# Optimization experiments

Measured on AMD Instinct MI355X. Metric: run time of the kernel, lower is better.

The kernel has to match this reference:

```python
import jax, jax.numpy as jnp
import numpy as np

NW, NT, F, H = 8192, 4096, 128, 128


def setup_inputs() -> dict:
    key = jax.random.key(0)
    ks = jax.random.split(key, 16)
    s = 1.0 / np.sqrt(F)
    sh = 1.0 / np.sqrt(H)
    inp = {
        "raw_worker_x": jax.random.normal(ks[0], (NW, F), jnp.float32),
        "raw_task_x": jax.random.normal(ks[1], (NT, F), jnp.float32),
        # sparse binary adjacencies (p=0.01), stored dense as the module expects
        "ww_adj": (jax.random.uniform(ks[2], (NW, NW)) < 0.01).astype(jnp.float32),
        "wt_adj": (jax.random.uniform(ks[3], (NW, NT)) < 0.01).astype(jnp.float32),
        # projections (Linear with bias), stored [in, out]
        "Wp_w": jax.random.uniform(ks[4], (F, H), jnp.float32, -s, s),
        "bp_w": jax.random.uniform(ks[5], (H,), jnp.float32, -s, s),
        "Wp_t": jax.random.uniform(ks[6], (F, H), jnp.float32, -s, s),
        "bp_t": jax.random.uniform(ks[7], (H,), jnp.float32, -s, s),
        # RGCN layer
        "W_worker": jax.random.uniform(ks[8], (H, H), jnp.float32, -sh, sh),
        "b_worker": jax.random.uniform(ks[9], (H,), jnp.float32, -sh, sh),
        "W_task": jax.random.uniform(ks[10], (H, H), jnp.float32, -sh, sh),
        "b_task": jax.random.uniform(ks[11], (H,), jnp.float32, -sh, sh),
        "W_ww": jax.random.uniform(ks[12], (H, H), jnp.float32, -sh, sh),
        "W_wt": jax.random.uniform(ks[13], (H, H), jnp.float32, -sh, sh),
        "W_tw": jax.random.uniform(ks[14], (H, H), jnp.float32, -sh, sh),
        # IGAT layer
        "W_igat": jax.random.uniform(ks[15], (H, H), jnp.float32, -sh, sh),
        "a_src": jax.random.normal(jax.random.fold_in(key, 100), (H, 1), jnp.float32) * 0.1,
        "a_dst": jax.random.normal(jax.random.fold_in(key, 101), (H, 1), jnp.float32) * 0.1,
    }
    return inp


def reference(raw_worker_x, raw_task_x, ww_adj, wt_adj,
              Wp_w, bp_w, Wp_t, bp_t,
              W_worker, b_worker, W_task, b_task,
              W_ww, W_wt, W_tw, W_igat, a_src, a_dst):
    # input projections
    h_w = jax.nn.relu(raw_worker_x @ Wp_w + bp_w)   # [NW, H]
    h_t = jax.nn.relu(raw_task_x @ Wp_t + bp_t)     # [NT, H]

    # HeteroRGCN layer
    ww_msg = ww_adj @ (h_w @ W_ww)                  # [NW, H]
    tw_msg = wt_adj @ (h_t @ W_tw)                  # [NW, H]
    wt_msg = wt_adj.T @ (h_w @ W_wt)                # [NT, H]
    h_w_rgcn = jax.nn.relu(h_w @ W_worker + b_worker + ww_msg + tw_msg)
    h_t_rgcn = jax.nn.relu(h_t @ W_task + b_task + wt_msg)

    # IGAT layer: dense masked attention over worker-worker graph
    Wh = h_w_rgcn @ W_igat                          # [NW, H]
    f_src = Wh @ a_src                              # [NW, 1]
    f_dst = Wh @ a_dst                              # [NW, 1]
    e = jax.nn.leaky_relu(f_src + f_dst.T, 0.2)     # [NW, NW]
    NEG = jnp.float32(-9e15)
    attn_logits = jnp.where(ww_adj > 0, e, NEG)
    attention = jax.nn.softmax(attn_logits, axis=-1)
    h_prime = jax.nn.elu(attention @ Wh)            # [NW, H]

    final_worker = h_prime + h_w
    final_task = h_t_rgcn + h_t
    return (final_worker, final_task)
```

## Files before the change

### kernel.cpp

```cpp
#include <hip/hip_runtime.h>

static constexpr int NWK  = 8192;
static constexpr int NTK  = 4096;
static constexpr int HD   = 128;
static constexpr int CWW  = 256;
static constexpr int CWTR = 128;
static constexpr int CWTC = 256;
static constexpr int QCW  = 128;
static constexpr int QCT  = 64;

typedef float  f32x4  __attribute__((ext_vector_type(4)));
typedef __bf16 bf16x8 __attribute__((ext_vector_type(8)));

__device__ __forceinline__ float b2f(unsigned short u){
  unsigned int x = ((unsigned int)u) << 16;
  return __builtin_bit_cast(float, x);
}
__device__ __forceinline__ unsigned short f2b(float x){
  return __builtin_bit_cast(unsigned short, (__bf16)x);
}
__device__ __forceinline__ float wredmax(float v){
#pragma unroll
  for(int o=32;o;o>>=1) v = fmaxf(v, __shfl_xor(v,o,64));
  return v;
}
__device__ __forceinline__ float wredsum(float v){
#pragma unroll
  for(int o=32;o;o>>=1) v += __shfl_xor(v,o,64);
  return v;
}

__global__ __launch_bounds__(256) void prepw(
    const float* s0,const float* s1,const float* s2,const float* s3,
    const float* s4,const float* s5,const float* s6,const float* s7,
    unsigned short* dst, int* fill, float* whsum){
  if(blockIdx.x < 16) fill[blockIdx.x*256 + threadIdx.x] = 0;
  if(blockIdx.x == 16 && threadIdx.x < 128) whsum[threadIdx.x] = 0.f;
  const float* srcs[8] = {s0,s1,s2,s3,s4,s5,s6,s7};
  int mat = blockIdx.x>>2, sl = blockIdx.x&3;
  const float* s = srcs[mat];
  unsigned short* d = dst + (size_t)mat*HD*HD;
  for(int idx=threadIdx.x + sl*4096; idx<(sl+1)*4096; idx+=256){
    int k = idx>>7, n = idx&127;
    d[n*HD+k] = f2b(s[idx]);
  }
}

template<int CAP>
__device__ __forceinline__ void scan_chunk(
    f32x4 x, int c0base, int& base, int* __restrict__ sbuf, int lane){
  bool p0=x.x>0.f, p1=x.y>0.f, p2=x.z>0.f, p3=x.w>0.f;
  unsigned long long b0=__ballot(p0),b1=__ballot(p1),b2=__ballot(p2),b3=__ballot(p3);
  unsigned long long below = (1ull<<lane)-1ull;
  int pos = base + __popcll(b0&below)+__popcll(b1&below)+__popcll(b2&below)+__popcll(b3&below);
  int c0 = c0base + lane*4;
  if(p0){ if(pos<CAP) sbuf[pos]=c0;   pos++; }
  if(p1){ if(pos<CAP) sbuf[pos]=c0+1; pos++; }
  if(p2){ if(pos<CAP) sbuf[pos]=c0+2; pos++; }
  if(p3){ if(pos<CAP) sbuf[pos]=c0+3; pos++; }
  base += __popcll(b0)+__popcll(b1)+__popcll(b2)+__popcll(b3);
}

template<int NCH, int QCAP, bool SCATTER>
__device__ __forceinline__ void scan_row_block(
    const float* __restrict__ adj, long row, int ncols, int cap,
    int* __restrict__ orow, int* __restrict__ deg,
    int* __restrict__ cidx, int* __restrict__ fill, int ccap,
    int lane, int w, int (* __restrict__ sbuf)[QCW], int* __restrict__ cnts){
  const int Q = NCH*256;
  const f32x4* src = (const f32x4*)(adj + row*(long)ncols) + ((w*Q)>>2);
  f32x4 v[NCH];
#pragma unroll
  for(int c=0;c<NCH;c++) v[c] = __builtin_nontemporal_load(&src[c*64 + lane]);
  int base = 0;
#pragma unroll
  for(int c=0;c<NCH;c++)
    scan_chunk<QCAP>(v[c], w*Q + c*256, base, sbuf[w], lane);
  int cnt = base<QCAP ? base : QCAP;
  if(lane==0) cnts[w] = cnt;
  __syncthreads();
  int c0=cnts[0], c1=cnts[1], c2=cnts[2], c3=cnts[3];
  int off = (w>0?c0:0) + (w>1?c1:0) + (w>2?c2:0);
  int tot = c0+c1+c2+c3;
  if(w==0 && lane==0) deg[row] = tot<cap ? tot : cap;
  for(int k=lane; k<cnt; k+=64){
    int p = off+k;
    if(p<cap) orow[p] = sbuf[w][k];
  }
  if(SCATTER){
    for(int k=lane; k<cnt; k+=64){
      int task = sbuf[w][k];
      int pp = atomicAdd(&fill[task], 1);
      if(pp < ccap) cidx[(long)task*ccap + pp] = (int)row;
    }
  }
}

__global__ __launch_bounds__(256) void build_all(
    const float* __restrict__ WW, const float* __restrict__ WT,
    int* __restrict__ ww_idx, int* __restrict__ ww_deg,
    int* __restrict__ wt_idx, int* __restrict__ wt_deg,
    int* __restrict__ cidx, int* __restrict__ fill){
  __shared__ int sbuf[4][QCW];
  __shared__ int cnts[4];
  int lane = threadIdx.x&63, w = threadIdx.x>>6;
  int b = blockIdx.x;
  if(b < NWK){
    long row = b;
    scan_row_block<8,QCW,false>(WW, row, NWK, CWW, ww_idx + row*CWW, ww_deg,
                                nullptr, nullptr, 0, lane, w, sbuf, cnts);
  } else {
    long row = b - NWK;
    scan_row_block<4,QCT,true>(WT, row, NTK, CWTR, wt_idx + row*CWTR, wt_deg,
                               cidx, fill, CWTC, lane, w, sbuf, cnts);
  }
}

__global__ __launch_bounds__(256) void kproj(
    const float* __restrict__ Xw, const float* __restrict__ Xt,
    const unsigned short* __restrict__ Wtb,
    const float* __restrict__ bp_w, const float* __restrict__ bp_t,
    unsigned short* __restrict__ h_w, unsigned short* __restrict__ h_t){
  bool task = blockIdx.x >= (NWK/32);
  const float* X = task ? Xt : Xw;
  const __bf16* Wt = (const __bf16*)(Wtb + (size_t)(task?1:0)*HD*HD);
  const float* bias = task ? bp_t : bp_w;
  unsigned short* H = task ? h_t : h_w;
  long r0 = (long)(task ? blockIdx.x-(NWK/32) : blockIdx.x)*32;

  __shared__ __bf16 As[32*HD];
  char* Ab = (char*)As;
  int t = threadIdx.x, lane = t&63, w = t>>6;
  const float4* A4 = (const float4*)(X + r0*HD);
#pragma unroll
  for(int i=0;i<4;i++){
    int id = t + i*256;
    float4 v = A4[id];
    int row = id>>5, c4 = id&31;
    int byte = row*256 + c4*8;
    ushort4 b; b.x=f2b(v.x); b.y=f2b(v.y); b.z=f2b(v.z); b.w=f2b(v.w);
    *(ushort4*)(Ab + (byte ^ ((row&7)<<4))) = b;
  }
  __syncthreads();
  f32x4 acc[2][2] = {};
  int n0 = w*32;
#pragma unroll
  for(int kk=0;kk<4;kk++){
    int kb = kk*32 + (lane>>4)*8;
    bf16x8 bf0 = *(const bf16x8*)(Wt + (n0 +      (lane&15))*HD + kb);
    bf16x8 bf1 = *(const bf16x8*)(Wt + (n0 + 16 + (lane&15))*HD + kb);
#pragma unroll
    for(int m=0;m<2;m++){
      int row = m*16 + (lane&15);
      bf16x8 af = *(const bf16x8*)(Ab + ((row*256 + kb*2) ^ ((row&7)<<4)));
      acc[m][0] = __builtin_amdgcn_mfma_f32_16x16x32_bf16(af, bf0, acc[m][0], 0,0,0);
      acc[m][1] = __builtin_amdgcn_mfma_f32_16x16x32_bf16(af, bf1, acc[m][1], 0,0,0);
    }
  }
#pragma unroll
  for(int m=0;m<2;m++)
#pragma unroll
  for(int n=0;n<2;n++){
    int col = n0 + n*16 + (lane&15);
    float bc = bias[col];
#pragma unroll
    for(int i=0;i<4;i++){
      long row = r0 + m*16 + (lane>>4)*4 + i;
      float vv = acc[m][n][i] + bc;
      vv = vv>0.f ? vv : 0.f;
      H[row*HD+col] = f2b(vv);
    }
  }
}

__device__ __forceinline__ void gather_sum(
    const unsigned short* __restrict__ tab, const int* __restrict__ ji, int d,
    int lane, float& ax, float& ay){
  int k=0;
  for(; k+3<d; k+=4){
    long j0=ji[k], j1=ji[k+1], j2=ji[k+2], j3=ji[k+3];
    ushort2 u0 = *(const ushort2*)(tab + j0*HD + lane*2);
    ushort2 u1 = *(const ushort2*)(tab + j1*HD + lane*2);
    ushort2 u2 = *(const ushort2*)(tab + j2*HD + lane*2);
    ushort2 u3 = *(const ushort2*)(tab + j3*HD + lane*2);
    ax += (b2f(u0.x)+b2f(u1.x)) + (b2f(u2.x)+b2f(u3.x));
    ay += (b2f(u0.y)+b2f(u1.y)) + (b2f(u2.y)+b2f(u3.y));
  }
  for(; k<d; ++k){
    long j0=ji[k];
    ushort2 u0 = *(const ushort2*)(tab + j0*HD + lane*2);
    ax += b2f(u0.x); ay += b2f(u0.y);
  }
}

__global__ __launch_bounds__(256) void agg(
    const unsigned short* __restrict__ h_w, const unsigned short* __restrict__ h_t,
    const int* __restrict__ wwidx, const int* __restrict__ wwdeg,
    const int* __restrict__ wtidx, const int* __restrict__ wtdeg,
    const int* __restrict__ cidx,  const int* __restrict__ fill,
    unsigned short* __restrict__ g_ww, unsigned short* __restrict__ g_tw,
    unsigned short* __restrict__ g_wt){
  int w = threadIdx.x>>6, lane = threadIdx.x&63;
  long i = (long)blockIdx.x*4 + w;
  if(i < NWK){
    float ax=0.f, ay=0.f;
    gather_sum(h_w, wwidx + i*CWW, wwdeg[i], lane, ax, ay);
    ushort2 o; o.x=f2b(ax); o.y=f2b(ay);
    *(ushort2*)(g_ww + i*HD + lane*2) = o;
    ax=0.f; ay=0.f;
    gather_sum(h_t, wtidx + i*CWTR, wtdeg[i], lane, ax, ay);
    o.x=f2b(ax); o.y=f2b(ay);
    *(ushort2*)(g_tw + i*HD + lane*2) = o;
  } else {
    long tt = i - NWK;
    float ax=0.f, ay=0.f;
    int d = fill[tt]; if(d>CWTC) d=CWTC;
    gather_sum(h_w, cidx + tt*CWTC, d, lane, ax, ay);
    ushort2 o; o.x=f2b(ax); o.y=f2b(ay);
    *(ushort2*)(g_wt + tt*HD + lane*2) = o;
  }
}

__device__ __forceinline__ void stage_bf16(char* Ab, const unsigned short* src, int t){
#pragma unroll
  for(int i=0;i<2;i++){
    int id = t + i*256;
    int row = id>>4, c8 = id&15;
    bf16x8 v = *(const bf16x8*)(src + row*HD + c8*8);
    int byte = row*256 + c8*16;
    *(bf16x8*)(Ab + (byte ^ ((row&7)<<4))) = v;
  }
}

__global__ __launch_bounds__(256) void krgcn(
    const unsigned short* __restrict__ h_w, const unsigned short* __restrict__ h_t,
    const unsigned short* __restrict__ g_ww, const unsigned short* __restrict__ g_tw,
    const unsigned short* __restrict__ g_wt,
    const unsigned short* __restrict__ Wtb,
    const float* __restrict__ b_worker, const float* __restrict__ b_task,
    const float* __restrict__ a_src, const float* __restrict__ a_dst,
    unsigned short* __restrict__ Wh, float* __restrict__ fs, float* __restrict__ fd,
    float* __restrict__ whsum, float* __restrict__ out_task){
  __shared__ __bf16 As[3][32*HD];
  __shared__ __bf16 Hs[32*HD];
  __shared__ float fsp[32][4], fdp[32][4];
  int t = threadIdx.x, lane = t&63, w = t>>6, n0 = w*32;
  bool task = blockIdx.x >= (NWK/32);

  if(!task){
    long r0 = (long)blockIdx.x*32;
    stage_bf16((char*)As[0], h_w  + r0*HD, t);
    stage_bf16((char*)As[1], g_ww + r0*HD, t);
    stage_bf16((char*)As[2], g_tw + r0*HD, t);
    __syncthreads();
    f32x4 acc[2][2] = {};
    const int slot[3] = {2,4,6};
#pragma unroll
    for(int s=0;s<3;s++){
      const __bf16* Wt = (const __bf16*)(Wtb + (size_t)slot[s]*HD*HD);
      char* Ab = (char*)As[s];
#pragma unroll
      for(int kk=0;kk<4;kk++){
        int kb = kk*32 + (lane>>4)*8;
        bf16x8 bf0 = *(const bf16x8*)(Wt + (n0 +      (lane&15))*HD + kb);
        bf16x8 bf1 = *(const bf16x8*)(Wt + (n0 + 16 + (lane&15))*HD + kb);
#pragma unroll
        for(int m=0;m<2;m++){
          int row = m*16 + (lane&15);
          bf16x8 af = *(const bf16x8*)(Ab + ((row*256 + kb*2) ^ ((row&7)<<4)));
          acc[m][0] = __builtin_amdgcn_mfma_f32_16x16x32_bf16(af, bf0, acc[m][0], 0,0,0);
          acc[m][1] = __builtin_amdgcn_mfma_f32_16x16x32_bf16(af, bf1, acc[m][1], 0,0,0);
        }
      }
    }
    char* HsB = (char*)Hs;
#pragma unroll
    for(int m=0;m<2;m++)
#pragma unroll
    for(int n=0;n<2;n++){
      int col = n0 + n*16 + (lane&15);
      float bc = b_worker[col];
#pragma unroll
      for(int i=0;i<4;i++){
        int row = m*16 + (lane>>4)*4 + i;
        float vv = acc[m][n][i] + bc;
        vv = vv>0.f ? vv : 0.f;
        int byte = row*256 + col*2;
        *(__bf16*)(HsB + (byte ^ ((row&7)<<4))) = (__bf16)vv;
      }
    }
    __syncthreads();
    f32x4 acc2[2][2] = {};
    const __bf16* Wt7 = (const __bf16*)(Wtb + (size_t)7*HD*HD);
#pragma unroll
    for(int kk=0;kk<4;kk++){
      int kb = kk*32 + (lane>>4)*8;
      bf16x8 bf0 = *(const bf16x8*)(Wt7 + (n0 +      (lane&15))*HD + kb);
      bf16x8 bf1 = *(const bf16x8*)(Wt7 + (n0 + 16 + (lane&15))*HD + kb);
#pragma unroll
      for(int m=0;m<2;m++){
        int row = m*16 + (lane&15);
        bf16x8 af = *(const bf16x8*)(HsB + ((row*256 + kb*2) ^ ((row&7)<<4)));
        acc2[m][0] = __builtin_amdgcn_mfma_f32_16x16x32_bf16(af, bf0, acc2[m][0], 0,0,0);
        acc2[m][1] = __builtin_amdgcn_mfma_f32_16x16x32_bf16(af, bf1, acc2[m][1], 0,0,0);
      }
    }
#pragma unroll
    for(int m=0;m<2;m++)
#pragma unroll
    for(int n=0;n<2;n++){
      int col = n0 + n*16 + (lane&15);
#pragma unroll
      for(int i=0;i<4;i++){
        long row = r0 + m*16 + (lane>>4)*4 + i;
        Wh[row*HD+col] = f2b(acc2[m][n][i]);
      }
    }
    float as0 = a_src[n0 + (lane&15)], as1 = a_src[n0 + 16 + (lane&15)];
    float ad0 = a_dst[n0 + (lane&15)], ad1 = a_dst[n0 + 16 + (lane&15)];
#pragma unroll
    for(int m=0;m<2;m++)
#pragma unroll
    for(int i=0;i<4;i++){
      float ps = acc2[m][0][i]*as0 + acc2[m][1][i]*as1;
      float pd = acc2[m][0][i]*ad0 + acc2[m][1][i]*ad1;
#pragma unroll
      for(int o=1;o<16;o<<=1){ ps += __shfl_xor(ps,o,64); pd += __shfl_xor(pd,o,64); }
      if((lane&15)==0){
        int row = m*16 + (lane>>4)*4 + i;
        fsp[row][w] = ps; fdp[row][w] = pd;
      }
    }
    float c0=0.f, c1=0.f;
#pragma unroll
    for(int m=0;m<2;m++)
#pragma unroll
    for(int i=0;i<4;i++){ c0 += acc2[m][0][i]; c1 += acc2[m][1][i]; }
    c0 += __shfl_xor(c0,16,64); c0 += __shfl_xor(c0,32,64);
    c1 += __shfl_xor(c1,16,64); c1 += __shfl_xor(c1,32,64);
    if(lane<16){
      atomicAdd(&whsum[n0+lane],    c0);
      atomicAdd(&whsum[n0+16+lane], c1);
    }
    __syncthreads();
    if(t < 32){
      fs[r0+t] = fsp[t][0]+fsp[t][1]+fsp[t][2]+fsp[t][3];
      fd[r0+t] = fdp[t][0]+fdp[t][1]+fdp[t][2]+fdp[t][3];
    }
  } else {
    long r0 = (long)(blockIdx.x - (NWK/32))*32;
    stage_bf16((char*)As[0], h_t  + r0*HD, t);
    stage_bf16((char*)As[1], g_wt + r0*HD, t);
    __syncthreads();
    f32x4 acc[2][2] = {};
    const int slot[2] = {3,5};
#pragma unroll
    for(int s=0;s<2;s++){
      const __bf16* Wt = (const __bf16*)(Wtb + (size_t)slot[s]*HD*HD);
      char* Ab = (char*)As[s];
#pragma unroll
      for(int kk=0;kk<4;kk++){
        int kb = kk*32 + (lane>>4)*8;
        bf16x8 bf0 = *(const bf16x8*)(Wt + (n0 +      (lane&15))*HD + kb);
        bf16x8 bf1 = *(const bf16x8*)(Wt + (n0 + 16 + (lane&15))*HD + kb);
#pragma unroll
        for(int m=0;m<2;m++){
          int row = m*16 + (lane&15);
          bf16x8 af = *(const bf16x8*)(Ab + ((row*256 + kb*2) ^ ((row&7)<<4)));
          acc[m][0] = __builtin_amdgcn_mfma_f32_16x16x32_bf16(af, bf0, acc[m][0], 0,0,0);
          acc[m][1] = __builtin_amdgcn_mfma_f32_16x16x32_bf16(af, bf1, acc[m][1], 0,0,0);
        }
      }
    }
#pragma unroll
    for(int m=0;m<2;m++)
#pragma unroll
    for(int n=0;n<2;n++){
      int col = n0 + n*16 + (lane&15);
      float bc = b_task[col];
#pragma unroll
      for(int i=0;i<4;i++){
        long row = r0 + m*16 + (lane>>4)*4 + i;
        float vv = acc[m][n][i] + bc;
        vv = vv>0.f ? vv : 0.f;
        vv += b2f(h_t[row*HD+col]);
        out_task[row*HD+col] = vv;
      }
    }
  }
}

__global__ __launch_bounds__(256) void attn(
    const unsigned short* __restrict__ Wh, const float* __restrict__ fs,
    const float* __restrict__ fd, const int* __restrict__ idx,
    const int* __restrict__ deg, const unsigned short* __restrict__ h_w,
    const float* __restrict__ whsum, float* __restrict__ out){
  __shared__ float pa[4][CWW];
  __shared__ int   pj[4][CWW];
  int w = threadIdx.x>>6, lane = threadIdx.x&63;
  long i = (long)blockIdx.x*4 + w;
  int d = deg[i];
  const int* ji = idx + i*CWW;
  float ax=0.f, ay=0.f;
  if(d > 0){
    float fsi = fs[i];
    float m = -1e30f;
    for(int k=lane;k<d;k+=64){
      int j = ji[k]; pj[w][k] = j;
      float e = fsi + fd[j];
      e = e>0.f ? e : 0.2f*e;
      pa[w][k] = e;
      m = fmaxf(m, e);
    }
    m = wredmax(m);
    float ssum = 0.f;
    for(int k=lane;k<d;k+=64){
      float e = __expf(pa[w][k]-m);
      pa[w][k] = e;
      ssum += e;
    }
    ssum = wredsum(ssum);
    float inv = 1.f/ssum;
    int k=0;
    for(; k+3<d; k+=4){
      float a0=pa[w][k], a1=pa[w][k+1], a2=pa[w][k+2], a3=pa[w][k+3];
      long j0=pj[w][k], j1=pj[w][k+1], j2=pj[w][k+2], j3=pj[w][k+3];
      ushort2 u0 = *(const ushort2*)(Wh + j0*HD + lane*2);
      ushort2 u1 = *(const ushort2*)(Wh + j1*HD + lane*2);
      ushort2 u2 = *(const ushort2*)(Wh + j2*HD + lane*2);
      ushort2 u3 = *(const ushort2*)(Wh + j3*HD + lane*2);
      ax += (a0*b2f(u0.x) + a1*b2f(u1.x)) + (a2*b2f(u2.x) + a3*b2f(u3.x));
      ay += (a0*b2f(u0.y) + a1*b2f(u1.y)) + (a2*b2f(u2.y) + a3*b2f(u3.y));
    }
    for(; k<d; ++k){
      float a0 = pa[w][k];
      long j0 = pj[w][k];
      ushort2 u0 = *(const ushort2*)(Wh + j0*HD + lane*2);
      ax += a0*b2f(u0.x);
      ay += a0*b2f(u0.y);
    }
    ax *= inv; ay *= inv;
  } else {
    ax = whsum[lane*2]   * (1.f/8192.f);
    ay = whsum[lane*2+1] * (1.f/8192.f);
  }
  ushort2 r = *(const ushort2*)(h_w + i*HD + lane*2);
  float2 o;
  o.x = (ax>0.f ? ax : __expf(ax)-1.f) + b2f(r.x);
  o.y = (ay>0.f ? ay : __expf(ay)-1.f) + b2f(r.y);
  *(float2*)(out + i*HD + lane*2) = o;
}

extern "C" void kernel_launch(void* const* d_in, const int* in_sizes, int n_in,
                              void* d_out, int out_size, void* d_ws, size_t ws_size,
                              hipStream_t stream){
  const float* Xw       = (const float*)d_in[0];
  const float* Xt       = (const float*)d_in[1];
  const float* WW       = (const float*)d_in[2];
  const float* WT       = (const float*)d_in[3];
  const float* Wp_w     = (const float*)d_in[4];
  const float* bp_w     = (const float*)d_in[5];
  const float* Wp_t     = (const float*)d_in[6];
  const float* bp_t     = (const float*)d_in[7];
  const float* W_worker = (const float*)d_in[8];
  const float* b_worker = (const float*)d_in[9];
  const float* W_task   = (const float*)d_in[10];
  const float* b_task   = (const float*)d_in[11];
  const float* W_ww     = (const float*)d_in[12];
  const float* W_wt     = (const float*)d_in[13];
  const float* W_tw     = (const float*)d_in[14];
  const float* W_igat   = (const float*)d_in[15];
  const float* a_src    = (const float*)d_in[16];
  const float* a_dst    = (const float*)d_in[17];
  float* out = (float*)d_out;

  char* p = (char*)d_ws;
  auto alloc = [&](size_t bytes)->char*{
    char* r = p; p += (bytes + 255) & ~(size_t)255; return r;
  };
  int* ww_idx  = (int*)alloc((size_t)NWK*CWW*4);
  int* wt_idx  = (int*)alloc((size_t)NWK*CWTR*4);
  int* wt_cidx = (int*)alloc((size_t)NTK*CWTC*4);
  int* ww_deg  = (int*)alloc(NWK*4);
  int* wt_deg  = (int*)alloc(NWK*4);
  int*   fill  = (int*)alloc(NTK*4);
  float* whsum = (float*)alloc(512);
  float* fs    = (float*)alloc(NWK*4);
  float* fd    = (float*)alloc(NWK*4);
  unsigned short* h_w  = (unsigned short*)alloc((size_t)NWK*HD*2);
  unsigned short* h_t  = (unsigned short*)alloc((size_t)NTK*HD*2);
  unsigned short* g_ww = (unsigned short*)alloc((size_t)NWK*HD*2);
  unsigned short* g_tw = (unsigned short*)alloc((size_t)NWK*HD*2);
  unsigned short* g_wt = (unsigned short*)alloc((size_t)NTK*HD*2);
  unsigned short* Wh   = (unsigned short*)alloc((size_t)NWK*HD*2);
  unsigned short* Wtb  = (unsigned short*)alloc((size_t)8*HD*HD*2);

  prepw<<<32,256,0,stream>>>(Wp_w, Wp_t, W_worker, W_task, W_ww, W_wt, W_tw, W_igat,
                             Wtb, fill, whsum);
  build_all<<<NWK*2,256,0,stream>>>(WW, WT, ww_idx, ww_deg, wt_idx, wt_deg,
                                    wt_cidx, fill);
  kproj<<<NWK/32 + NTK/32,256,0,stream>>>(Xw, Xt, Wtb, bp_w, bp_t, h_w, h_t);
  agg<<<(NWK+NTK)/4,256,0,stream>>>(h_w, h_t, ww_idx, ww_deg, wt_idx, wt_deg,
                                    wt_cidx, fill, g_ww, g_tw, g_wt);
  krgcn<<<NWK/32 + NTK/32,256,0,stream>>>(h_w, h_t, g_ww, g_tw, g_wt, Wtb,
                                          b_worker, b_task, a_src, a_dst,
                                          Wh, fs, fd, whsum, out + (size_t)NWK*HD);
  attn<<<NWK/4,256,0,stream>>>(Wh, fs, fd, ww_idx, ww_deg, h_w, whsum, out);
}
```

Measured before the change: 154.1 us.

## Fuse adjacency scan and input projection into one launch, two rows per block

Merges the adjacency-to-index build kernel and the input projection GEMM kernel into a single launch, with projection blocks first and scan blocks after. Each scan block now processes two adjacency rows, issuing both rows' nontemporal loads up front to raise memory-level parallelism and halve the block count. This removes a kernel launch boundary and lets projection work overlap with the bandwidth-bound scan. The cost is larger shared memory per block, since the scan buffers and the projection tile are both allocated, which may reduce occupancy for the scan blocks.

```diff
diff --git a/kernel.cpp b/kernel.cpp
--- a/kernel.cpp
+++ b/kernel.cpp
@@ -8,6 +8,7 @@
 static constexpr int CWTC = 256;
 static constexpr int QCW  = 128;
 static constexpr int QCT  = 64;
+static constexpr int KPB  = NWK/32 + NTK/32;
 
 typedef float  f32x4  __attribute__((ext_vector_type(4)));
 typedef __bf16 bf16x8 __attribute__((ext_vector_type(8)));
@@ -62,73 +63,85 @@
 }
 
 template<int NCH, int QCAP, bool SCATTER>
-__device__ __forceinline__ void scan_row_block(
-    const float* __restrict__ adj, long row, int ncols, int cap,
-    int* __restrict__ orow, int* __restrict__ deg,
+__device__ __forceinline__ void scan_row_pair(
+    const float* __restrict__ adj, long rowA, int ncols, int cap,
+    int* __restrict__ idx, int* __restrict__ deg,
     int* __restrict__ cidx, int* __restrict__ fill, int ccap,
-    int lane, int w, int (* __restrict__ sbuf)[QCW], int* __restrict__ cnts){
+    int lane, int w, int (* __restrict__ sbufA)[QCW], int (* __restrict__ sbufB)[QCW],
+    int* __restrict__ cntsA, int* __restrict__ cntsB){
+  long rowB = rowA + 1;
   const int Q = NCH*256;
-  const f32x4* src = (const f32x4*)(adj + row*(long)ncols) + ((w*Q)>>2);
-  f32x4 v[NCH];
-#pragma unroll
-  for(int c=0;c<NCH;c++) v[c] = __builtin_nontemporal_load(&src[c*64 + lane]);
-  int base = 0;
+  const f32x4* srcA = (const f32x4*)(adj + rowA*(long)ncols) + ((w*Q)>>2);
+  const f32x4* srcB = (const f32x4*)(adj + rowB*(long)ncols) + ((w*Q)>>2);
+  f32x4 vA[NCH], vB[NCH];
+#pragma unroll
+  for(int c=0;c<NCH;c++) vA[c] = __builtin_nontemporal_load(&srcA[c*64 + lane]);
+#pragma unroll
+  for(int c=0;c<NCH;c++) vB[c] = __builtin_nontemporal_load(&srcB[c*64 + lane]);
+  int baseA = 0;
 #pragma unroll
   for(int c=0;c<NCH;c++)
-    scan_chunk<QCAP>(v[c], w*Q + c*256, base, sbuf[w], lane);
-  int cnt = base<QCAP ? base : QCAP;
-  if(lane==0) cnts[w] = cnt;
+    scan_chunk<QCAP>(vA[c], w*Q + c*256, baseA, sbufA[w], lane);
+  int cntA = baseA<QCAP ? baseA : QCAP;
+  if(lane==0) cntsA[w] = cntA;
+  int baseB = 0;
+#pragma unroll
+  for(int c=0;c<NCH;c++)
+    scan_chunk<QCAP>(vB[c], w*Q + c*256, baseB, sbufB[w], lane);
+  int cntB = baseB<QCAP ? baseB : QCAP;
+  if(lane==0) cntsB[w] = cntB;
   __syncthreads();
-  int c0=cnts[0], c1=cnts[1], c2=cnts[2], c3=cnts[3];
-  int off = (w>0?c0:0) + (w>1?c1:0) + (w>2?c2:0);
-  int tot = c0+c1+c2+c3;
-  if(w==0 && lane==0) deg[row] = tot<cap ? tot : cap;
-  for(int k=lane; k<cnt; k+=64){
-    int p = off+k;
-    if(p<cap) orow[p] = sbuf[w][k];
-  }
-  if(SCATTER){
-    for(int k=lane; k<cnt; k+=64){
-      int task = sbuf[w][k];
-      int pp = atomicAdd(&fill[task], 1);
-      if(pp < ccap) cidx[(long)task*ccap + pp] = (int)row;
-    }
-  }
-}
-
-__global__ __launch_bounds__(256) void build_all(
-    const float* __restrict__ WW, const float* __restrict__ WT,
-    int* __restrict__ ww_idx, int* __restrict__ ww_deg,
-    int* __restrict__ wt_idx, int* __restrict__ wt_deg,
-    int* __restrict__ cidx, int* __restrict__ fill){
-  __shared__ int sbuf[4][QCW];
-  __shared__ int cnts[4];
-  int lane = threadIdx.x&63, w = threadIdx.x>>6;
-  int b = blockIdx.x;
-  if(b < NWK){
-    long row = b;
-    scan_row_block<8,QCW,false>(WW, row, NWK, CWW, ww_idx + row*CWW, ww_deg,
-                                nullptr, nullptr, 0, lane, w, sbuf, cnts);
-  } else {
-    long row = b - NWK;
-    scan_row_block<4,QCT,true>(WT, row, NTK, CWTR, wt_idx + row*CWTR, wt_deg,
-                               cidx, fill, CWTC, lane, w, sbuf, cnts);
-  }
-}
-
-__global__ __launch_bounds__(256) void kproj(
-    const float* __restrict__ Xw, const float* __restrict__ Xt,
+  {
+    int c0=cntsA[0], c1=cntsA[1], c2=cntsA[2], c3=cntsA[3];
+    int off = (w>0?c0:0) + (w>1?c1:0) + (w>2?c2:0);
+    int tot = c0+c1+c2+c3;
+    if(w==0 && lane==0) deg[rowA] = tot<cap ? tot : cap;
+    int* orow = idx + rowA*(long)cap;
+    for(int k=lane; k<cntA; k+=64){
+      int p = off+k;
+      if(p<cap) orow[p] = sbufA[w][k];
+    }
+    if(SCATTER){
+      for(int k=lane; k<cntA; k+=64){
+        int task = sbufA[w][k];
+        int pp = atomicAdd(&fill[task], 1);
+        if(pp < ccap) cidx[(long)task*ccap + pp] = (int)rowA;
+      }
+    }
+  }
+  {
+    int c0=cntsB[0], c1=cntsB[1], c2=cntsB[2], c3=cntsB[3];
+    int off = (w>0?c0:0) + (w>1?c1:0) + (w>2?c2:0);
+    int tot = c0+c1+c2+c3;
+    if(w==0 && lane==0) deg[rowB] = tot<cap ? tot : cap;
+    int* orow = idx + rowB*(long)cap;
+    for(int k=lane; k<cntB; k+=64){
+      int p = off+k;
+      if(p<cap) orow[p] = sbufB[w][k];
+    }
+    if(SCATTER){
+      for(int k=lane; k<cntB; k+=64){
+        int task = sbufB[w][k];
+        int pp = atomicAdd(&fill[task], 1);
+        if(pp < ccap) cidx[(long)task*ccap + pp] = (int)rowB;
+      }
+    }
+  }
+}
+
+__device__ __forceinline__ void kproj_body(
+    int bk, const float* __restrict__ Xw, const float* __restrict__ Xt,
     const unsigned short* __restrict__ Wtb,
     const float* __restrict__ bp_w, const float* __restrict__ bp_t,
-    unsigned short* __restrict__ h_w, unsigned short* __restrict__ h_t){
-  bool task = blockIdx.x >= (NWK/32);
+    unsigned short* __restrict__ h_w, unsigned short* __restrict__ h_t,
+    __bf16* As){
+  bool task = bk >= (NWK/32);
   const float* X = task ? Xt : Xw;
   const __bf16* Wt = (const __bf16*)(Wtb + (size_t)(task?1:0)*HD*HD);
   const float* bias = task ? bp_t : bp_w;
   unsigned short* H = task ? h_t : h_w;
-  long r0 = (long)(task ? blockIdx.x-(NWK/32) : blockIdx.x)*32;
-
-  __shared__ __bf16 As[32*HD];
+  long r0 = (long)(task ? bk-(NWK/32) : bk)*32;
+
   char* Ab = (char*)As;
   int t = threadIdx.x, lane = t&63, w = t>>6;
   const float4* A4 = (const float4*)(X + r0*HD);
@@ -170,6 +183,34 @@
       vv = vv>0.f ? vv : 0.f;
       H[row*HD+col] = f2b(vv);
     }
+  }
+}
+
+__global__ __launch_bounds__(256) void fused_front(
+    const float* __restrict__ WW, const float* __restrict__ WT,
+    int* __restrict__ ww_idx, int* __restrict__ ww_deg,
+    int* __restrict__ wt_idx, int* __restrict__ wt_deg,
+    int* __restrict__ cidx, int* __restrict__ fill,
+    const float* __restrict__ Xw, const float* __restrict__ Xt,
+    const unsigned short* __restrict__ Wtb,
+    const float* __restrict__ bp_w, const float* __restrict__ bp_t,
+    unsigned short* __restrict__ h_w, unsigned short* __restrict__ h_t){
+  __shared__ int sbufA[4][QCW];
+  __shared__ int sbufB[4][QCW];
+  __shared__ int cntsA[4], cntsB[4];
+  __shared__ __bf16 As[32*HD];
+  int lane = threadIdx.x&63, w = threadIdx.x>>6;
+  int b = blockIdx.x;
+  if(b < KPB){
+    kproj_body(b, Xw, Xt, Wtb, bp_w, bp_t, h_w, h_t, As);
+  } else if(b < KPB + NWK/2){
+    long rowA = (long)(b - KPB)*2;
+    scan_row_pair<8,QCW,false>(WW, rowA, NWK, CWW, ww_idx, ww_deg,
+                               nullptr, nullptr, 0, lane, w, sbufA, sbufB, cntsA, cntsB);
+  } else {
+    long rowA = (long)(b - KPB - NWK/2)*2;
+    scan_row_pair<4,QCT,true>(WT, rowA, NTK, CWTR, wt_idx, wt_deg,
+                              cidx, fill, CWTC, lane, w, sbufA, sbufB, cntsA, cntsB);
   }
 }
 
@@ -497,9 +538,9 @@
 
   prepw<<<32,256,0,stream>>>(Wp_w, Wp_t, W_worker, W_task, W_ww, W_wt, W_tw, W_igat,
                              Wtb, fill, whsum);
-  build_all<<<NWK*2,256,0,stream>>>(WW, WT, ww_idx, ww_deg, wt_idx, wt_deg,
-                                    wt_cidx, fill);
-  kproj<<<NWK/32 + NTK/32,256,0,stream>>>(Xw, Xt, Wtb, bp_w, bp_t, h_w, h_t);
+  fused_front<<<KPB + NWK,256,0,stream>>>(WW, WT, ww_idx, ww_deg, wt_idx, wt_deg,
+                                          wt_cidx, fill, Xw, Xt, Wtb, bp_w, bp_t,
+                                          h_w, h_t);
   agg<<<(NWK+NTK)/4,256,0,stream>>>(h_w, h_t, ww_idx, ww_deg, wt_idx, wt_deg,
                                     wt_cidx, fill, g_ww, g_tw, g_wt);
   krgcn<<<NWK/32 + NTK/32,256,0,stream>>>(h_w, h_t, g_ww, g_tw, g_wt, Wtb,
```

Measured after the change: 157.9 us. 2.5% more time.

## Fuse row-wise neighbor aggregation into adjacency scan kernel

Applied to the files above, without the earlier changes.

Moves kproj before the adjacency scan so the scan kernel can gather and sum neighbor features for ww and tw rows straight from its shared-memory index buffer. Partial sums from the four waves are reduced in LDS and written out. This removes the separate agg pass over those rows and its re-read of the index arrays. Only the column-wise wt aggregation stays in a smaller kernel. The risk is that the build kernel now stalls on random gathers while holding adjacency loads in flight, and ww rows with more than 128 neighbors in one wave slice are truncated in the sum, as they already were in the stored indices.

```diff
diff --git a/kernel.cpp b/kernel.cpp
--- a/kernel.cpp
+++ b/kernel.cpp
@@ -46,6 +46,26 @@
   }
 }
 
+__device__ __forceinline__ void gather_sum(
+    const unsigned short* __restrict__ tab, const int* __restrict__ ji, int d,
+    int lane, float& ax, float& ay){
+  int k=0;
+  for(; k+3<d; k+=4){
+    long j0=ji[k], j1=ji[k+1], j2=ji[k+2], j3=ji[k+3];
+    ushort2 u0 = *(const ushort2*)(tab + j0*HD + lane*2);
+    ushort2 u1 = *(const ushort2*)(tab + j1*HD + lane*2);
+    ushort2 u2 = *(const ushort2*)(tab + j2*HD + lane*2);
+    ushort2 u3 = *(const ushort2*)(tab + j3*HD + lane*2);
+    ax += (b2f(u0.x)+b2f(u1.x)) + (b2f(u2.x)+b2f(u3.x));
+    ay += (b2f(u0.y)+b2f(u1.y)) + (b2f(u2.y)+b2f(u3.y));
+  }
+  for(; k<d; ++k){
+    long j0=ji[k];
+    ushort2 u0 = *(const ushort2*)(tab + j0*HD + lane*2);
+    ax += b2f(u0.x); ay += b2f(u0.y);
+  }
+}
+
 template<int CAP>
 __device__ __forceinline__ void scan_chunk(
     f32x4 x, int c0base, int& base, int* __restrict__ sbuf, int lane){
@@ -66,7 +86,10 @@
     const float* __restrict__ adj, long row, int ncols, int cap,
     int* __restrict__ orow, int* __restrict__ deg,
     int* __restrict__ cidx, int* __restrict__ fill, int ccap,
-    int lane, int w, int (* __restrict__ sbuf)[QCW], int* __restrict__ cnts){
+    const unsigned short* __restrict__ htab, unsigned short* __restrict__ grow,
+    int lane, int w, int tid,
+    int (* __restrict__ sbuf)[QCW], float (* __restrict__ gpart)[HD],
+    int* __restrict__ cnts){
   const int Q = NCH*256;
   const f32x4* src = (const f32x4*)(adj + row*(long)ncols) + ((w*Q)>>2);
   f32x4 v[NCH];
@@ -78,6 +101,10 @@
     scan_chunk<QCAP>(v[c], w*Q + c*256, base, sbuf[w], lane);
   int cnt = base<QCAP ? base : QCAP;
   if(lane==0) cnts[w] = cnt;
+  float ax=0.f, ay=0.f;
+  gather_sum(htab, sbuf[w], cnt, lane, ax, ay);
+  gpart[w][lane*2]   = ax;
+  gpart[w][lane*2+1] = ay;
   __syncthreads();
   int c0=cnts[0], c1=cnts[1], c2=cnts[2], c3=cnts[3];
   int off = (w>0?c0:0) + (w>1?c1:0) + (w>2?c2:0);
@@ -87,6 +114,10 @@
     int p = off+k;
     if(p<cap) orow[p] = sbuf[w][k];
   }
+  if(tid < 128){
+    float s = gpart[0][tid]+gpart[1][tid]+gpart[2][tid]+gpart[3][tid];
+    grow[tid] = f2b(s);
+  }
   if(SCATTER){
     for(int k=lane; k<cnt; k+=64){
       int task = sbuf[w][k];
@@ -100,19 +131,24 @@
     const float* __restrict__ WW, const float* __restrict__ WT,
     int* __restrict__ ww_idx, int* __restrict__ ww_deg,
     int* __restrict__ wt_idx, int* __restrict__ wt_deg,
-    int* __restrict__ cidx, int* __restrict__ fill){
-  __shared__ int sbuf[4][QCW];
-  __shared__ int cnts[4];
-  int lane = threadIdx.x&63, w = threadIdx.x>>6;
+    int* __restrict__ cidx, int* __restrict__ fill,
+    const unsigned short* __restrict__ h_w, const unsigned short* __restrict__ h_t,
+    unsigned short* __restrict__ g_ww, unsigned short* __restrict__ g_tw){
+  __shared__ int   sbuf[4][QCW];
+  __shared__ float gpart[4][HD];
+  __shared__ int   cnts[4];
+  int lane = threadIdx.x&63, w = threadIdx.x>>6, tid = threadIdx.x;
   int b = blockIdx.x;
   if(b < NWK){
     long row = b;
     scan_row_block<8,QCW,false>(WW, row, NWK, CWW, ww_idx + row*CWW, ww_deg,
-                                nullptr, nullptr, 0, lane, w, sbuf, cnts);
+                                nullptr, nullptr, 0, h_w, g_ww + row*HD,
+                                lane, w, tid, sbuf, gpart, cnts);
   } else {
     long row = b - NWK;
     scan_row_block<4,QCT,true>(WT, row, NTK, CWTR, wt_idx + row*CWTR, wt_deg,
-                               cidx, fill, CWTC, lane, w, sbuf, cnts);
+                               cidx, fill, CWTC, h_t, g_tw + row*HD,
+                               lane, w, tid, sbuf, gpart, cnts);
   }
 }
 
@@ -173,52 +209,16 @@
   }
 }
 
-__device__ __forceinline__ void gather_sum(
-    const unsigned short* __restrict__ tab, const int* __restrict__ ji, int d,
-    int lane, float& ax, float& ay){
-  int k=0;
-  for(; k+3<d; k+=4){
-    long j0=ji[k], j1=ji[k+1], j2=ji[k+2], j3=ji[k+3];
-    ushort2 u0 = *(const ushort2*)(tab + j0*HD + lane*2);
-    ushort2 u1 = *(const ushort2*)(tab + j1*HD + lane*2);
-    ushort2 u2 = *(const ushort2*)(tab + j2*HD + lane*2);
-    ushort2 u3 = *(const ushort2*)(tab + j3*HD + lane*2);
-    ax += (b2f(u0.x)+b2f(u1.x)) + (b2f(u2.x)+b2f(u3.x));
-    ay += (b2f(u0.y)+b2f(u1.y)) + (b2f(u2.y)+b2f(u3.y));
-  }
-  for(; k<d; ++k){
-    long j0=ji[k];
-    ushort2 u0 = *(const ushort2*)(tab + j0*HD + lane*2);
-    ax += b2f(u0.x); ay += b2f(u0.y);
-  }
-}
-
-__global__ __launch_bounds__(256) void agg(
-    const unsigned short* __restrict__ h_w, const unsigned short* __restrict__ h_t,
-    const int* __restrict__ wwidx, const int* __restrict__ wwdeg,
-    const int* __restrict__ wtidx, const int* __restrict__ wtdeg,
-    const int* __restrict__ cidx,  const int* __restrict__ fill,
-    unsigned short* __restrict__ g_ww, unsigned short* __restrict__ g_tw,
-    unsigned short* __restrict__ g_wt){
+__global__ __launch_bounds__(256) void agg_csc(
+    const unsigned short* __restrict__ h_w, const int* __restrict__ cidx,
+    const int* __restrict__ fill, unsigned short* __restrict__ g_wt){
   int w = threadIdx.x>>6, lane = threadIdx.x&63;
-  long i = (long)blockIdx.x*4 + w;
-  if(i < NWK){
-    float ax=0.f, ay=0.f;
-    gather_sum(h_w, wwidx + i*CWW, wwdeg[i], lane, ax, ay);
-    ushort2 o; o.x=f2b(ax); o.y=f2b(ay);
-    *(ushort2*)(g_ww + i*HD + lane*2) = o;
-    ax=0.f; ay=0.f;
-    gather_sum(h_t, wtidx + i*CWTR, wtdeg[i], lane, ax, ay);
-    o.x=f2b(ax); o.y=f2b(ay);
-    *(ushort2*)(g_tw + i*HD + lane*2) = o;
-  } else {
-    long tt = i - NWK;
-    float ax=0.f, ay=0.f;
-    int d = fill[tt]; if(d>CWTC) d=CWTC;
-    gather_sum(h_w, cidx + tt*CWTC, d, lane, ax, ay);
-    ushort2 o; o.x=f2b(ax); o.y=f2b(ay);
-    *(ushort2*)(g_wt + tt*HD + lane*2) = o;
-  }
+  long tt = (long)blockIdx.x*4 + w;
+  float ax=0.f, ay=0.f;
+  int d = fill[tt]; if(d>CWTC) d=CWTC;
+  gather_sum(h_w, cidx + tt*CWTC, d, lane, ax, ay);
+  ushort2 o; o.x=f2b(ax); o.y=f2b(ay);
+  *(ushort2*)(g_wt + tt*HD + lane*2) = o;
 }
 
 __device__ __forceinline__ void stage_bf16(char* Ab, const unsigned short* src, int t){
@@ -497,11 +497,10 @@
 
   prepw<<<32,256,0,stream>>>(Wp_w, Wp_t, W_worker, W_task, W_ww, W_wt, W_tw, W_igat,
                              Wtb, fill, whsum);
+  kproj<<<NWK/32 + NTK/32,256,0,stream>>>(Xw, Xt, Wtb, bp_w, bp_t, h_w, h_t);
   build_all<<<NWK*2,256,0,stream>>>(WW, WT, ww_idx, ww_deg, wt_idx, wt_deg,
-                                    wt_cidx, fill);
-  kproj<<<NWK/32 + NTK/32,256,0,stream>>>(Xw, Xt, Wtb, bp_w, bp_t, h_w, h_t);
-  agg<<<(NWK+NTK)/4,256,0,stream>>>(h_w, h_t, ww_idx, ww_deg, wt_idx, wt_deg,
-                                    wt_cidx, fill, g_ww, g_tw, g_wt);
+                                    wt_cidx, fill, h_w, h_t, g_ww, g_tw);
+  agg_csc<<<NTK/4,256,0,stream>>>(h_w, wt_cidx, fill, g_wt);
   krgcn<<<NWK/32 + NTK/32,256,0,stream>>>(h_w, h_t, g_ww, g_tw, g_wt, Wtb,
                                           b_worker, b_task, a_src, a_dst,
                                           Wh, fs, fd, whsum, out + (size_t)NWK*HD);
```

Measured after the change: 144.3 us, median of 2. -6.4%, faster.
